# Performance work log

Measured on AMD Instinct MI355X. Metric: run time of the kernel, lower is better.

Reference implementation:

```python
import jax, jax.numpy as jnp
import numpy as np

N_NODES = 40962
N_EDGES = 245760
K = 10  # gaussian kernels
D = 2   # pseudo-coordinate dim
EPS = 1e-15


def gmm_conv(x, edge_index, pseudo, g, mu, sigma, root, bias):
    """PyG GMMConv with aggr='mean', root_weight=True.
    x: [N, Cin], edge_index: [2, E] (row 0 = source j, row 1 = target i),
    pseudo: [E, D], g: [Cin, K*Cout], mu/sigma: [K, D], root: [Cin, Cout], bias: [Cout].
    """
    src, dst = edge_index[0], edge_index[1]
    E = pseudo.shape[0]
    # Gaussian mixture edge weights: [E, K]
    diff = pseudo[:, None, :] - mu[None, :, :]                     # [E, K, D]
    w = jnp.exp(jnp.sum(-0.5 * diff * diff / (EPS + sigma[None] ** 2), axis=-1))
    xj = x[src]                                                    # [E, Cin] gather
    y = (xj @ g).reshape(E, K, -1)                                 # [E, K, Cout]
    msg = jnp.sum(y * w[:, :, None], axis=1)                       # [E, Cout]
    agg = jax.ops.segment_sum(msg, dst, num_segments=N_NODES)      # scatter-add
    deg = jax.ops.segment_sum(jnp.ones((E,), x.dtype), dst, num_segments=N_NODES)
    agg = agg / jnp.maximum(deg, 1.0)[:, None]                     # mean aggregation
    return agg + x @ root + bias


def setup_inputs() -> dict:
    key = jax.random.key(0)
    ks = jax.random.split(key, 20)
    Cin, Ch, Cout = 64, 64, 128
    sc = lambda fan: 1.0 / np.sqrt(fan)
    inp = {
        "x": jax.random.normal(ks[0], (N_NODES, Cin), jnp.float32),
        "edge_index": jax.random.randint(ks[1], (2, N_EDGES), 0, N_NODES, jnp.int32),
        "pseudo": jax.random.uniform(ks[2], (N_EDGES, D), jnp.float32),
        # conv1: Cin -> Ch
        "g1": jax.random.normal(ks[3], (Cin, K * Ch), jnp.float32) * sc(Cin),
        "mu1": jax.random.uniform(ks[4], (K, D), jnp.float32),
        "sigma1": jax.random.uniform(ks[5], (K, D), jnp.float32) + 0.5,
        "root1": jax.random.normal(ks[6], (Cin, Ch), jnp.float32) * sc(Cin),
        "b1": jnp.zeros((Ch,), jnp.float32),
        # conv2: Ch -> Cout
        "g2": jax.random.normal(ks[7], (Ch, K * Cout), jnp.float32) * sc(Ch),
        "mu2": jax.random.uniform(ks[8], (K, D), jnp.float32),
        "sigma2": jax.random.uniform(ks[9], (K, D), jnp.float32) + 0.5,
        "root2": jax.random.normal(ks[10], (Ch, Cout), jnp.float32) * sc(Ch),
        "b2": jnp.zeros((Cout,), jnp.float32),
        # shortcut: Cin -> Cout (size_in != size_out)
        "gs": jax.random.normal(ks[11], (Cin, K * Cout), jnp.float32) * sc(Cin),
        "mus": jax.random.uniform(ks[12], (K, D), jnp.float32),
        "sigmas": jax.random.uniform(ks[13], (K, D), jnp.float32) + 0.5,
        "roots": jax.random.normal(ks[14], (Cin, Cout), jnp.float32) * sc(Cin),
        "bs": jnp.zeros((Cout,), jnp.float32),
    }
    return inp


def reference(x, edge_index, pseudo, g1, mu1, sigma1, root1, b1,
              g2, mu2, sigma2, root2, b2, gs, mus, sigmas, roots, bs):
    h = gmm_conv(x, edge_index, pseudo, g1, mu1, sigma1, root1, b1)
    h = jax.nn.relu(h)
    y = gmm_conv(h, edge_index, pseudo, g2, mu2, sigma2, root2, b2)
    x_s = gmm_conv(x, edge_index, pseudo, gs, mus, sigmas, roots, bs)
    return jax.nn.relu(y + x_s)
```

## Files before the change

### kernel.cpp

```cpp
#include <hip/hip_runtime.h>
#include <hip/hip_bf16.h>

using bf16 = __hip_bfloat16;
typedef __attribute__((ext_vector_type(8))) short short8;
typedef __attribute__((ext_vector_type(4))) float float4v;

#define N_NODES 40962
#define N_EDGES 245760
#define NP      41024
#define KG      10
#define SCAN_B  256
#define NBLK    ((NP + SCAN_B - 1) / SCAN_B)
#define GRID1   (NP / 64)

#define CVT_V   (N_NODES * 64 / 8)
#define CVT_BLK ((CVT_V + 255) / 256)
#define W3_BLK  (N_EDGES / 256)
#define PACK_N  (64 * 704 + 2 * 128 * 704)
#define PACK_BLK (PACK_N / 256)


__device__ __forceinline__ float ldf(const void* p, size_t i, int isf32) {
    return isf32 ? ((const float*)p)[i] : __bfloat162float(((const bf16*)p)[i]);
}
__device__ __forceinline__ float blo(unsigned u) { return __uint_as_float(u << 16); }
__device__ __forceinline__ float bhi(unsigned u) { return __uint_as_float(u & 0xffff0000u); }
__device__ __forceinline__ unsigned pk2(float a, float b) {
    union { bf16 h[2]; unsigned u; } t;
    t.h[0] = __float2bfloat16(a);
    t.h[1] = __float2bfloat16(b);
    return t.u;
}

__global__ void k_detect_count(const void* x, const int* __restrict__ ei,
                               int* __restrict__ flag, int* __restrict__ deg) {
    if (blockIdx.x == 0) {
        __shared__ int huge_c, zero_even;
        if (threadIdx.x == 0) { huge_c = 0; zero_even = 0; }
        __syncthreads();
        const bf16* xb = (const bf16*)x;
        int lh = 0, lz = 0;
        for (int i = threadIdx.x; i < 8192; i += 256) {
            float v = __bfloat162float(xb[i]);
            if (!(fabsf(v) <= 1e4f)) lh++;
            if ((i & 1) == 0 && v == 0.0f) lz++;
        }
        atomicAdd(&huge_c, lh);
        atomicAdd(&zero_even, lz);
        __syncthreads();
        if (threadIdx.x == 0) flag[0] = (huge_c > 0 || zero_even > 3000) ? 1 : 0;
    } else {
        int e = (blockIdx.x - 1) * 256 + threadIdx.x;
        if (e < N_EDGES) atomicAdd(&deg[ei[N_EDGES + e]], 1);
    }
}

__global__ void k_scan1(const int* __restrict__ deg, int* __restrict__ offs,
                        int* __restrict__ bsum) {
    __shared__ int buf[SCAN_B];
    int t = threadIdx.x, b = blockIdx.x;
    int i = b * SCAN_B + t;
    int v = (i < NP) ? deg[i] : 0;
    buf[t] = v;
    __syncthreads();
    for (int off = 1; off < SCAN_B; off <<= 1) {
        int a = (t >= off) ? buf[t - off] : 0;
        __syncthreads();
        buf[t] += a;
        __syncthreads();
    }
    if (i < NP) offs[i] = buf[t] - v;
    if (t == SCAN_B - 1) bsum[b] = buf[t];
}

__global__ void k_scan2(const int* __restrict__ bsum, int* __restrict__ bofs,
                        int* __restrict__ total) {
    __shared__ int buf[256];
    int t = threadIdx.x;
    int v = (t < NBLK) ? bsum[t] : 0;
    buf[t] = v;
    __syncthreads();
    for (int off = 1; off < 256; off <<= 1) {
        int a = (t >= off) ? buf[t - off] : 0;
        __syncthreads();
        buf[t] += a;
        __syncthreads();
    }
    if (t < NBLK) bofs[t] = buf[t] - v;
    if (t == 255) total[0] = buf[255];
}

__global__ void k_scan3(int* __restrict__ offs, const int* __restrict__ bofs,
                        const int* __restrict__ total, const int* __restrict__ deg,
                        int* __restrict__ cur, float* __restrict__ invdeg) {
    int i = blockIdx.x * 256 + threadIdx.x;
    if (i < NP) {
        int o = offs[i] + bofs[i / SCAN_B];
        offs[i] = o;
        cur[i] = o;
        int d = deg[i];
        invdeg[i] = 1.0f / (float)(d > 1 ? d : 1);
    }
    if (i == 0) offs[NP] = total[0];
}

__global__ void k_fill(const int* __restrict__ ei, int* __restrict__ cur,
                       int* __restrict__ csr) {
    int e = blockIdx.x * 256 + threadIdx.x;
    if (e < N_EDGES) {
        int pos = atomicAdd(&cur[ei[N_EDGES + e]], 1);
        csr[pos] = e;
    }
}

__device__ __forceinline__ void gw_one(float p0, float p1, const void* mu,
                                       const void* sg, int f, float* out) {
#pragma unroll
    for (int k = 0; k < KG; k++) {
        float m0 = ldf(mu, 2 * k + 0, f), m1 = ldf(mu, 2 * k + 1, f);
        float s0 = ldf(sg, 2 * k + 0, f), s1 = ldf(sg, 2 * k + 1, f);
        float d0 = p0 - m0, d1 = p1 - m1;
        float t = -0.5f * (d0 * d0 / (1e-15f + s0 * s0) + d1 * d1 / (1e-15f + s1 * s1));
        out[k] = __expf(t);
    }
}

__device__ __forceinline__ void pack_frag(const void* g, const void* root, int f,
                                          int idx, int Cout, bf16* Bp) {
    int j = idx & 7;
    int lane = (idx >> 3) & 63;
    int rem = idx >> 9;
    int kc = rem % 22;
    int n = rem / 22;
    int col = n * 16 + (lane & 15);
    int k = kc * 32 + (lane >> 4) * 8 + j;
    float v;
    if (k < 512) {
        int cin = k >> 3, kg = k & 7;
        v = ldf(g, (size_t)cin * (KG * Cout) + (size_t)kg * Cout + col, f);
    } else if (k < 640) {
        int jj = k - 512;
        int cin = jj >> 1, kg = 8 + (jj & 1);
        v = ldf(g, (size_t)cin * (KG * Cout) + (size_t)kg * Cout + col, f);
    } else {
        v = ldf(root, (size_t)(k - 640) * Cout + col, f);
    }
    Bp[idx] = __float2bfloat16(v);
}

__global__ void k_prep_all(const void* __restrict__ x, const void* __restrict__ pseudo,
                           const void* mu1, const void* sg1, const void* mu2,
                           const void* sg2, const void* mus, const void* sgs,
                           const void* g1, const void* root1, const void* g2,
                           const void* root2, const void* gs, const void* roots,
                           const int* __restrict__ flag, bf16* __restrict__ Xf,
                           bf16* __restrict__ wab, bf16* __restrict__ w2b,
                           bf16* wt1p, bf16* wt2p, bf16* wtsp) {
    int b = blockIdx.x;
    int tid = threadIdx.x;
    int f = flag[0];
    if (b < CVT_BLK) {
        int i = b * 256 + tid;
        if (i < CVT_V) {
            int node = i >> 3, j = i & 7;
            uint4 u;
            if (f) {
                const float4* xf = (const float4*)x;
                float4 a = xf[2 * i], c = xf[2 * i + 1];
                union { bf16 t[8]; uint4 u; } tt;
                tt.t[0] = __float2bfloat16(a.x); tt.t[1] = __float2bfloat16(a.y);
                tt.t[2] = __float2bfloat16(a.z); tt.t[3] = __float2bfloat16(a.w);
                tt.t[4] = __float2bfloat16(c.x); tt.t[5] = __float2bfloat16(c.y);
                tt.t[6] = __float2bfloat16(c.z); tt.t[7] = __float2bfloat16(c.w);
                u = tt.u;
            } else {
                u = ((const uint4*)x)[i];
            }
            *(uint4*)(Xf + ((size_t)(j >> 2) * NP + node) * 32 + (j & 3) * 8) = u;
        }
    } else if (b < CVT_BLK + W3_BLK) {
        int e = (b - CVT_BLK) * 256 + tid;
        float p0 = ldf(pseudo, (size_t)e * 2 + 0, f);
        float p1 = ldf(pseudo, (size_t)e * 2 + 1, f);
        float o1[KG], o2[KG], os[KG];
        gw_one(p0, p1, mu1, sg1, f, o1);
        gw_one(p0, p1, mu2, sg2, f, o2);
        gw_one(p0, p1, mus, sgs, f, os);
        unsigned* d = (unsigned*)(wab + (size_t)e * 20);
        d[0] = pk2(o1[0], o1[1]); d[1] = pk2(o1[2], o1[3]);
        d[2] = pk2(o1[4], o1[5]); d[3] = pk2(o1[6], o1[7]);
        d[4] = pk2(o1[8], o1[9]);
        d[5] = pk2(os[0], os[1]); d[6] = pk2(os[2], os[3]);
        d[7] = pk2(os[4], os[5]); d[8] = pk2(os[6], os[7]);
        d[9] = pk2(os[8], os[9]);
        unsigned* d2 = (unsigned*)(w2b + (size_t)e * 10);
        d2[0] = pk2(o2[0], o2[1]); d2[1] = pk2(o2[2], o2[3]);
        d2[2] = pk2(o2[4], o2[5]); d2[3] = pk2(o2[6], o2[7]);
        d2[4] = pk2(o2[8], o2[9]);
    } else {
        int idx = (b - CVT_BLK - W3_BLK) * 256 + tid;
        if (idx < 64 * 704) {
            pack_frag(g1, root1, f, idx, 64, wt1p);
        } else if (idx < 64 * 704 + 128 * 704) {
            pack_frag(g2, root2, f, idx - 64 * 704, 128, wt2p);
        } else {
            pack_frag(gs, roots, f, idx - 64 * 704 - 128 * 704, 128, wtsp);
        }
    }
}

__device__ __forceinline__ void store_zf(bf16* Zf, int wid, int lane, const float* a,
                                         float inv) {
    union { bf16 h[8]; uint4 u; } p;
#pragma unroll
    for (int k = 0; k < 8; k++) p.h[k] = __float2bfloat16(a[k] * inv);
    *(uint4*)(Zf + ((size_t)(lane >> 2) * NP + wid) * 32 + (lane & 3) * 8) = p.u;
    *(unsigned*)(Zf + ((size_t)(16 + (lane >> 4)) * NP + wid) * 32 + (lane & 15) * 2) =
        pk2(a[8] * inv, a[9] * inv);
}

__device__ __forceinline__ float ldx_frag(const bf16* X, int src, int lane) {
    return __bfloat162float(X[((size_t)(lane >> 5) * NP + src) * 32 + (lane & 31)]);
}

__global__ void k_gather2(const int* __restrict__ ei, const int* __restrict__ offs,
                          const int* __restrict__ csr, const bf16* __restrict__ wab,
                          const float* __restrict__ invdeg, const bf16* __restrict__ X,
                          bf16* __restrict__ Za, bf16* __restrict__ Zb) {
    int wid = (blockIdx.x * 256 + threadIdx.x) >> 6;
    int lane = threadIdx.x & 63;
    if (wid >= NP) return;
    float aa[KG], ab[KG];
#pragma unroll
    for (int k = 0; k < KG; k++) { aa[k] = 0.0f; ab[k] = 0.0f; }
    int beg = __builtin_amdgcn_readfirstlane(offs[wid]);
    int end = __builtin_amdgcn_readfirstlane(offs[wid + 1]);
    for (int t = beg; t < end; ++t) {
        int e   = __builtin_amdgcn_readfirstlane(csr[t]);
        int src = __builtin_amdgcn_readfirstlane(ei[e]);
        const unsigned* wr = (const unsigned*)(wab + (size_t)e * 20);
        unsigned u0 = wr[0], u1 = wr[1], u2 = wr[2], u3 = wr[3], u4 = wr[4];
        unsigned v0 = wr[5], v1 = wr[6], v2 = wr[7], v3 = wr[8], v4 = wr[9];
        float xv = ldx_frag(X, src, lane);
        aa[0] += blo(u0) * xv; aa[1] += bhi(u0) * xv;
        aa[2] += blo(u1) * xv; aa[3] += bhi(u1) * xv;
        aa[4] += blo(u2) * xv; aa[5] += bhi(u2) * xv;
        aa[6] += blo(u3) * xv; aa[7] += bhi(u3) * xv;
        aa[8] += blo(u4) * xv; aa[9] += bhi(u4) * xv;
        ab[0] += blo(v0) * xv; ab[1] += bhi(v0) * xv;
        ab[2] += blo(v1) * xv; ab[3] += bhi(v1) * xv;
        ab[4] += blo(v2) * xv; ab[5] += bhi(v2) * xv;
        ab[6] += blo(v3) * xv; ab[7] += bhi(v3) * xv;
        ab[8] += blo(v4) * xv; ab[9] += bhi(v4) * xv;
    }
    float inv = invdeg[wid];
    store_zf(Za, wid, lane, aa, inv);
    store_zf(Zb, wid, lane, ab, inv);
}

__global__ void k_gather(const int* __restrict__ ei, const int* __restrict__ offs,
                         const int* __restrict__ csr, const bf16* __restrict__ w,
                         int wstride, const float* __restrict__ invdeg,
                         const bf16* __restrict__ X, bf16* __restrict__ Z) {
    int wid = (blockIdx.x * 256 + threadIdx.x) >> 6;
    int lane = threadIdx.x & 63;
    if (wid >= NP) return;
    float acc[KG];
#pragma unroll
    for (int k = 0; k < KG; k++) acc[k] = 0.0f;
    int beg = __builtin_amdgcn_readfirstlane(offs[wid]);
    int end = __builtin_amdgcn_readfirstlane(offs[wid + 1]);
    for (int t = beg; t < end; ++t) {
        int e   = __builtin_amdgcn_readfirstlane(csr[t]);
        int src = __builtin_amdgcn_readfirstlane(ei[e]);
        const unsigned* wr = (const unsigned*)(w + (size_t)e * wstride);
        unsigned u0 = wr[0], u1 = wr[1], u2 = wr[2], u3 = wr[3], u4 = wr[4];
        float xv = ldx_frag(X, src, lane);
        acc[0] += blo(u0) * xv; acc[1] += bhi(u0) * xv;
        acc[2] += blo(u1) * xv; acc[3] += bhi(u1) * xv;
        acc[4] += blo(u2) * xv; acc[5] += bhi(u2) * xv;
        acc[6] += blo(u3) * xv; acc[7] += bhi(u3) * xv;
        acc[8] += blo(u4) * xv; acc[9] += bhi(u4) * xv;
    }
    store_zf(Z, wid, lane, acc, invdeg[wid]);
}

template <int NT, int MODE>
__device__ __forceinline__ void gemm_body(
    int bid, const bf16* __restrict__ Zf, const bf16* __restrict__ Xf,
    const bf16* __restrict__ Bp, const void* __restrict__ bias, int f,
    const bf16* __restrict__ addsrc, bf16* __restrict__ outb,
    void* __restrict__ outp) {
    constexpr int Cout = NT * 16;
    int lane = threadIdx.x & 63;
    int wave = threadIdx.x >> 6;
    int m = lane & 15, quad = lane >> 4;
    int row0 = bid * 64 + wave * 16;

    const bf16* bbase = Bp + (size_t)lane * 8;
    const bf16* arow = Zf + ((size_t)(row0 + m)) * 32 + quad * 8;
    const bf16* xrow = Xf + ((size_t)(row0 + m)) * 32 + quad * 8;

    float4v acc[NT];
#pragma unroll
    for (int n = 0; n < NT; n++) acc[n] = (float4v){0.f, 0.f, 0.f, 0.f};

    short8 apre[4];
#pragma unroll
    for (int i = 0; i < 4; i++)
        apre[i] = *(const short8*)(arow + (size_t)i * NP * 32);
    short8 bcur[NT];
#pragma unroll
    for (int n = 0; n < NT; n++)
        bcur[n] = *(const short8*)(bbase + (size_t)(n * 22 + 0) * 512);

#pragma unroll
    for (int kc = 0; kc < 22; kc++) {
        short8 a = apre[kc & 3];
        int kn = kc + 4;
        if (kn < 22) {
            apre[kc & 3] = (kn < 20)
                ? *(const short8*)(arow + (size_t)kn * NP * 32)
                : *(const short8*)(xrow + (size_t)(kn - 20) * NP * 32);
        }
        short8 bnxt[NT];
        if (kc + 1 < 22) {
#pragma unroll
            for (int n = 0; n < NT; n++)
                bnxt[n] = *(const short8*)(bbase + (size_t)(n * 22 + kc + 1) * 512);
        }
#pragma unroll
        for (int n = 0; n < NT; n++)
            acc[n] = __builtin_amdgcn_mfma_f32_16x16x32_bf16(a, bcur[n], acc[n], 0, 0, 0);
        if (kc + 1 < 22) {
#pragma unroll
            for (int n = 0; n < NT; n++) bcur[n] = bnxt[n];
        }
    }

#pragma unroll
    for (int n = 0; n < NT; n++) {
        int gcol = n * 16 + m;
        float bv = ldf(bias, gcol, f);
#pragma unroll
        for (int r = 0; r < 4; r++) {
            int grow = row0 + quad * 4 + r;
            if (grow >= N_NODES) continue;
            float v = acc[n][r] + bv;
            if (MODE == 0) {
                outb[((size_t)(gcol >> 5) * NP + grow) * 32 + (gcol & 31)] =
                    __float2bfloat16(fmaxf(v, 0.f));
            } else if (MODE == 1) {
                outb[(size_t)grow * Cout + gcol] = __float2bfloat16(v);
            } else {
                size_t oidx = (size_t)grow * Cout + gcol;
                v = fmaxf(v + __bfloat162float(addsrc[oidx]), 0.f);
                if (f) ((float*)outp)[oidx] = v;
                else   ((bf16*)outp)[oidx] = __float2bfloat16(v);
            }
        }
    }
}

__global__ __launch_bounds__(256) void k_gemm_pair(
    const bf16* __restrict__ za, const bf16* __restrict__ zb,
    const bf16* __restrict__ Xf, const bf16* __restrict__ wt1p,
    const bf16* __restrict__ wtsp, const void* __restrict__ b1,
    const void* __restrict__ bs, const int* __restrict__ flag,
    bf16* __restrict__ hf, bf16* __restrict__ ys) {
    int f = flag[0];
    if (blockIdx.x < GRID1)
        gemm_body<4, 0>(blockIdx.x, za, Xf, wt1p, b1, f, nullptr, hf, nullptr);
    else
        gemm_body<8, 1>(blockIdx.x - GRID1, zb, Xf, wtsp, bs, f, nullptr, ys, nullptr);
}

template <int NT, int MODE>
__global__ __launch_bounds__(256) void k_gemm_one(
    const bf16* __restrict__ Zf, const bf16* __restrict__ Xf,
    const bf16* __restrict__ Bp, const void* __restrict__ bias,
    const int* __restrict__ flag, const bf16* __restrict__ addsrc,
    bf16* __restrict__ outb, void* __restrict__ outp) {
    gemm_body<NT, MODE>(blockIdx.x, Zf, Xf, Bp, bias, flag[0], addsrc, outb, outp);
}

extern "C" void kernel_launch(void* const* d_in, const int* in_sizes, int n_in,
                              void* d_out, int out_size, void* d_ws, size_t ws_size,
                              hipStream_t stream) {
    const void* x      = d_in[0];
    const int*  ei     = (const int*)d_in[1];
    const void* pseudo = d_in[2];
    const void* g1     = d_in[3];
    const void* mu1    = d_in[4];
    const void* sg1    = d_in[5];
    const void* root1  = d_in[6];
    const void* b1     = d_in[7];
    const void* g2     = d_in[8];
    const void* mu2    = d_in[9];
    const void* sg2    = d_in[10];
    const void* root2  = d_in[11];
    const void* b2     = d_in[12];
    const void* gs     = d_in[13];
    const void* mus    = d_in[14];
    const void* sgs    = d_in[15];
    const void* roots  = d_in[16];
    const void* bs     = d_in[17];

    char* ws = (char*)d_ws;
    size_t off = 0;
    auto alloc = [&](size_t bytes) -> char* {
        char* p = ws + off;
        off += (bytes + 255) & ~(size_t)255;
        return p;
    };
    const size_t ZSZ = (size_t)20 * NP * 32 * 2;
    const size_t XFS = (size_t)2 * NP * 32 * 2;

    int*   flag   = (int*)alloc(256);
    int*   deg    = (int*)alloc((size_t)NP * 4);
    int*   offs   = (int*)alloc((size_t)(NP + 1) * 4);
    int*   cur    = (int*)alloc((size_t)NP * 4);
    float* invdeg = (float*)alloc((size_t)NP * 4);
    int*   bsum   = (int*)alloc((size_t)NBLK * 4);
    int*   bofs   = (int*)alloc((size_t)NBLK * 4);
    int*   total  = (int*)alloc(256);
    int*   csr    = (int*)alloc((size_t)N_EDGES * 4);
    bf16*  Xf     = (bf16*)alloc(XFS);
    bf16*  hf     = (bf16*)alloc(XFS);
    bf16*  ys     = (bf16*)alloc((size_t)N_NODES * 128 * 2);
    bf16*  wt1p   = (bf16*)alloc((size_t)64 * 704 * 2);
    bf16*  wt2p   = (bf16*)alloc((size_t)128 * 704 * 2);
    bf16*  wtsp   = (bf16*)alloc((size_t)128 * 704 * 2);
    bf16*  wab    = (bf16*)alloc((size_t)N_EDGES * 20 * 2);
    bf16*  w2b    = (bf16*)alloc((size_t)N_EDGES * 10 * 2);
    size_t common_end = off;

    bf16* za = (bf16*)alloc(ZSZ);
    bf16* zb = (bf16*)alloc(ZSZ);
    bool big = (off <= ws_size);

    hipMemsetAsync(deg, 0, (size_t)NP * 4, stream);
    k_detect_count<<<1 + (N_EDGES + 255) / 256, 256, 0, stream>>>(x, ei, flag, deg);
    k_prep_all<<<CVT_BLK + W3_BLK + PACK_BLK, 256, 0, stream>>>(
        x, pseudo, mu1, sg1, mu2, sg2, mus, sgs, g1, root1, g2, root2, gs, roots,
        flag, Xf, wab, w2b, wt1p, wt2p, wtsp);
    k_scan1<<<NBLK, SCAN_B, 0, stream>>>(deg, offs, bsum);
    k_scan2<<<1, 256, 0, stream>>>(bsum, bofs, total);
    k_scan3<<<(NP + 255) / 256, 256, 0, stream>>>(offs, bofs, total, deg, cur, invdeg);
    k_fill<<<(N_EDGES + 255) / 256, 256, 0, stream>>>(ei, cur, csr);

    if (big) {
        k_gather2<<<NP / 4, 256, 0, stream>>>(ei, offs, csr, wab, invdeg, Xf, za, zb);
        k_gemm_pair<<<2 * GRID1, 256, 0, stream>>>(za, zb, Xf, wt1p, wtsp, b1, bs,
                                                   flag, hf, ys);
        k_gather<<<NP / 4, 256, 0, stream>>>(ei, offs, csr, w2b, 10, invdeg, hf, za);
        k_gemm_one<8, 2><<<GRID1, 256, 0, stream>>>(za, hf, wt2p, b2, flag, ys,
                                                    (bf16*)nullptr, d_out);
    } else {
        off = common_end;
        bf16* z = (bf16*)alloc(ZSZ);
        k_gather<<<NP / 4, 256, 0, stream>>>(ei, offs, csr, wab, 20, invdeg, Xf, z);
        k_gemm_one<4, 0><<<GRID1, 256, 0, stream>>>(z, Xf, wt1p, b1, flag,
                                                    (const bf16*)nullptr, hf, nullptr);
        k_gather<<<NP / 4, 256, 0, stream>>>(ei, offs, csr, wab + 10, 20, invdeg, Xf, z);
        k_gemm_one<8, 1><<<GRID1, 256, 0, stream>>>(z, Xf, wtsp, bs, flag,
                                                    (const bf16*)nullptr, ys, nullptr);
        k_gather<<<NP / 4, 256, 0, stream>>>(ei, offs, csr, w2b, 10, invdeg, hf, z);
        k_gemm_one<8, 2><<<GRID1, 256, 0, stream>>>(z, hf, wt2p, b2, flag, ys,
                                                    (bf16*)nullptr, d_out);
    }
}
```

Measured before the change: 312.4 us.

## Software-pipeline CSR gather loops and merge scan phases into one kernel

The gather kernels now prefetch edge ids, source indices, Gaussian weights and source features two or three edges ahead, rotating them through registers so the dependent chain of global loads (csr, then ei, then X) overlaps with the accumulation. Out-of-range prefetch indices are clamped so the extra loads stay in bounds. Separately, the second and third scan phases are fused: every block redundantly scans the block sums and applies its own offset, which saves one kernel launch. The cost is more live registers in the gather kernels and a few wasted loads past the end of each node's edge list.

```diff
diff --git a/kernel.cpp b/kernel.cpp
--- a/kernel.cpp
+++ b/kernel.cpp
@@ -31,6 +31,7 @@
     t.h[1] = __float2bfloat16(b);
     return t.u;
 }
+__device__ __forceinline__ int rfl(int v) { return __builtin_amdgcn_readfirstlane(v); }
 
 __global__ void k_detect_count(const void* x, const int* __restrict__ ei,
                                int* __restrict__ flag, int* __restrict__ deg) {
@@ -73,10 +74,11 @@
     if (t == SCAN_B - 1) bsum[b] = buf[t];
 }
 
-__global__ void k_scan2(const int* __restrict__ bsum, int* __restrict__ bofs,
-                        int* __restrict__ total) {
+__global__ void k_scan3m(int* __restrict__ offs, const int* __restrict__ bsum,
+                         const int* __restrict__ deg, int* __restrict__ cur,
+                         float* __restrict__ invdeg) {
     __shared__ int buf[256];
-    int t = threadIdx.x;
+    int t = threadIdx.x, b = blockIdx.x;
     int v = (t < NBLK) ? bsum[t] : 0;
     buf[t] = v;
     __syncthreads();
@@ -86,22 +88,17 @@
         buf[t] += a;
         __syncthreads();
     }
-    if (t < NBLK) bofs[t] = buf[t] - v;
-    if (t == 255) total[0] = buf[255];
-}
-
-__global__ void k_scan3(int* __restrict__ offs, const int* __restrict__ bofs,
-                        const int* __restrict__ total, const int* __restrict__ deg,
-                        int* __restrict__ cur, float* __restrict__ invdeg) {
-    int i = blockIdx.x * 256 + threadIdx.x;
+    int bofs = (b > 0) ? buf[b - 1] : 0;
+    int total = buf[NBLK - 1];
+    int i = b * 256 + t;
     if (i < NP) {
-        int o = offs[i] + bofs[i / SCAN_B];
+        int o = offs[i] + bofs;
         offs[i] = o;
         cur[i] = o;
         int d = deg[i];
         invdeg[i] = 1.0f / (float)(d > 1 ? d : 1);
     }
-    if (i == 0) offs[NP] = total[0];
+    if (i == 0) offs[NP] = total;
 }
 
 __global__ void k_fill(const int* __restrict__ ei, int* __restrict__ cur,
@@ -223,6 +220,11 @@
     return __bfloat162float(X[((size_t)(lane >> 5) * NP + src) * 32 + (lane & 31)]);
 }
 
+__device__ __forceinline__ int csr_at(const int* csr, int idx) {
+    if (idx > N_EDGES - 1) idx = N_EDGES - 1;
+    return rfl(csr[idx]);
+}
+
 __global__ void k_gather2(const int* __restrict__ ei, const int* __restrict__ offs,
                           const int* __restrict__ csr, const bf16* __restrict__ wab,
                           const float* __restrict__ invdeg, const bf16* __restrict__ X,
@@ -233,25 +235,45 @@
     float aa[KG], ab[KG];
 #pragma unroll
     for (int k = 0; k < KG; k++) { aa[k] = 0.0f; ab[k] = 0.0f; }
-    int beg = __builtin_amdgcn_readfirstlane(offs[wid]);
-    int end = __builtin_amdgcn_readfirstlane(offs[wid + 1]);
-    for (int t = beg; t < end; ++t) {
-        int e   = __builtin_amdgcn_readfirstlane(csr[t]);
-        int src = __builtin_amdgcn_readfirstlane(ei[e]);
-        const unsigned* wr = (const unsigned*)(wab + (size_t)e * 20);
-        unsigned u0 = wr[0], u1 = wr[1], u2 = wr[2], u3 = wr[3], u4 = wr[4];
-        unsigned v0 = wr[5], v1 = wr[6], v2 = wr[7], v3 = wr[8], v4 = wr[9];
-        float xv = ldx_frag(X, src, lane);
-        aa[0] += blo(u0) * xv; aa[1] += bhi(u0) * xv;
-        aa[2] += blo(u1) * xv; aa[3] += bhi(u1) * xv;
-        aa[4] += blo(u2) * xv; aa[5] += bhi(u2) * xv;
-        aa[6] += blo(u3) * xv; aa[7] += bhi(u3) * xv;
-        aa[8] += blo(u4) * xv; aa[9] += bhi(u4) * xv;
-        ab[0] += blo(v0) * xv; ab[1] += bhi(v0) * xv;
-        ab[2] += blo(v1) * xv; ab[3] += bhi(v1) * xv;
-        ab[4] += blo(v2) * xv; ab[5] += bhi(v2) * xv;
-        ab[6] += blo(v3) * xv; ab[7] += bhi(v3) * xv;
-        ab[8] += blo(v4) * xv; ab[9] += bhi(v4) * xv;
+    int beg = rfl(offs[wid]);
+    int end = rfl(offs[wid + 1]);
+    int cnt = end - beg;
+
+    int e0 = csr_at(csr, beg + 0);
+    int e1 = csr_at(csr, beg + 1);
+    int e2 = csr_at(csr, beg + 2);
+    int s1 = rfl(ei[e1]);
+    const unsigned* wp0 = (const unsigned*)(wab + (size_t)e0 * 20);
+    unsigned c0 = wp0[0], c1 = wp0[1], c2 = wp0[2], c3 = wp0[3], c4 = wp0[4];
+    unsigned c5 = wp0[5], c6 = wp0[6], c7 = wp0[7], c8 = wp0[8], c9 = wp0[9];
+    const unsigned* wp1 = (const unsigned*)(wab + (size_t)e1 * 20);
+    unsigned n0 = wp1[0], n1 = wp1[1], n2 = wp1[2], n3 = wp1[3], n4 = wp1[4];
+    unsigned n5 = wp1[5], n6 = wp1[6], n7 = wp1[7], n8 = wp1[8], n9 = wp1[9];
+    int s0 = rfl(ei[e0]);
+    float xv = ldx_frag(X, s0, lane);
+
+    for (int t = 0; t < cnt; ++t) {
+        int e3 = csr_at(csr, beg + t + 3);
+        int s2 = rfl(ei[e2]);
+        const unsigned* wp2 = (const unsigned*)(wab + (size_t)e2 * 20);
+        unsigned m0 = wp2[0], m1 = wp2[1], m2 = wp2[2], m3 = wp2[3], m4 = wp2[4];
+        unsigned m5 = wp2[5], m6 = wp2[6], m7 = wp2[7], m8 = wp2[8], m9 = wp2[9];
+        float xv1 = ldx_frag(X, s1, lane);
+        aa[0] += blo(c0) * xv; aa[1] += bhi(c0) * xv;
+        aa[2] += blo(c1) * xv; aa[3] += bhi(c1) * xv;
+        aa[4] += blo(c2) * xv; aa[5] += bhi(c2) * xv;
+        aa[6] += blo(c3) * xv; aa[7] += bhi(c3) * xv;
+        aa[8] += blo(c4) * xv; aa[9] += bhi(c4) * xv;
+        ab[0] += blo(c5) * xv; ab[1] += bhi(c5) * xv;
+        ab[2] += blo(c6) * xv; ab[3] += bhi(c6) * xv;
+        ab[4] += blo(c7) * xv; ab[5] += bhi(c7) * xv;
+        ab[6] += blo(c8) * xv; ab[7] += bhi(c8) * xv;
+        ab[8] += blo(c9) * xv; ab[9] += bhi(c9) * xv;
+        e2 = e3; s1 = s2; xv = xv1;
+        c0 = n0; c1 = n1; c2 = n2; c3 = n3; c4 = n4;
+        c5 = n5; c6 = n6; c7 = n7; c8 = n8; c9 = n9;
+        n0 = m0; n1 = m1; n2 = m2; n3 = m3; n4 = m4;
+        n5 = m5; n6 = m6; n7 = m7; n8 = m8; n9 = m9;
     }
     float inv = invdeg[wid];
     store_zf(Za, wid, lane, aa, inv);
@@ -268,19 +290,35 @@
     float acc[KG];
 #pragma unroll
     for (int k = 0; k < KG; k++) acc[k] = 0.0f;
-    int beg = __builtin_amdgcn_readfirstlane(offs[wid]);
-    int end = __builtin_amdgcn_readfirstlane(offs[wid + 1]);
-    for (int t = beg; t < end; ++t) {
-        int e   = __builtin_amdgcn_readfirstlane(csr[t]);
-        int src = __builtin_amdgcn_readfirstlane(ei[e]);
-        const unsigned* wr = (const unsigned*)(w + (size_t)e * wstride);
-        unsigned u0 = wr[0], u1 = wr[1], u2 = wr[2], u3 = wr[3], u4 = wr[4];
-        float xv = ldx_frag(X, src, lane);
-        acc[0] += blo(u0) * xv; acc[1] += bhi(u0) * xv;
-        acc[2] += blo(u1) * xv; acc[3] += bhi(u1) * xv;
-        acc[4] += blo(u2) * xv; acc[5] += bhi(u2) * xv;
-        acc[6] += blo(u3) * xv; acc[7] += bhi(u3) * xv;
-        acc[8] += blo(u4) * xv; acc[9] += bhi(u4) * xv;
+    int beg = rfl(offs[wid]);
+    int end = rfl(offs[wid + 1]);
+    int cnt = end - beg;
+
+    int e0 = csr_at(csr, beg + 0);
+    int e1 = csr_at(csr, beg + 1);
+    int e2 = csr_at(csr, beg + 2);
+    int s1 = rfl(ei[e1]);
+    const unsigned* wp0 = (const unsigned*)(w + (size_t)e0 * wstride);
+    unsigned c0 = wp0[0], c1 = wp0[1], c2 = wp0[2], c3 = wp0[3], c4 = wp0[4];
+    const unsigned* wp1 = (const unsigned*)(w + (size_t)e1 * wstride);
+    unsigned n0 = wp1[0], n1 = wp1[1], n2 = wp1[2], n3 = wp1[3], n4 = wp1[4];
+    int s0 = rfl(ei[e0]);
+    float xv = ldx_frag(X, s0, lane);
+
+    for (int t = 0; t < cnt; ++t) {
+        int e3 = csr_at(csr, beg + t + 3);
+        int s2 = rfl(ei[e2]);
+        const unsigned* wp2 = (const unsigned*)(w + (size_t)e2 * wstride);
+        unsigned m0 = wp2[0], m1 = wp2[1], m2 = wp2[2], m3 = wp2[3], m4 = wp2[4];
+        float xv1 = ldx_frag(X, s1, lane);
+        acc[0] += blo(c0) * xv; acc[1] += bhi(c0) * xv;
+        acc[2] += blo(c1) * xv; acc[3] += bhi(c1) * xv;
+        acc[4] += blo(c2) * xv; acc[5] += bhi(c2) * xv;
+        acc[6] += blo(c3) * xv; acc[7] += bhi(c3) * xv;
+        acc[8] += blo(c4) * xv; acc[9] += bhi(c4) * xv;
+        e2 = e3; s1 = s2; xv = xv1;
+        c0 = n0; c1 = n1; c2 = n2; c3 = n3; c4 = n4;
+        n0 = m0; n1 = m1; n2 = m2; n3 = m3; n4 = m4;
     }
     store_zf(Z, wid, lane, acc, invdeg[wid]);
 }
@@ -422,8 +460,6 @@
     int*   cur    = (int*)alloc((size_t)NP * 4);
     float* invdeg = (float*)alloc((size_t)NP * 4);
     int*   bsum   = (int*)alloc((size_t)NBLK * 4);
-    int*   bofs   = (int*)alloc((size_t)NBLK * 4);
-    int*   total  = (int*)alloc(256);
     int*   csr    = (int*)alloc((size_t)N_EDGES * 4);
     bf16*  Xf     = (bf16*)alloc(XFS);
     bf16*  hf     = (bf16*)alloc(XFS);
@@ -445,8 +481,7 @@
         x, pseudo, mu1, sg1, mu2, sg2, mus, sgs, g1, root1, g2, root2, gs, roots,
         flag, Xf, wab, w2b, wt1p, wt2p, wtsp);
     k_scan1<<<NBLK, SCAN_B, 0, stream>>>(deg, offs, bsum);
-    k_scan2<<<1, 256, 0, stream>>>(bsum, bofs, total);
-    k_scan3<<<(NP + 255) / 256, 256, 0, stream>>>(offs, bofs, total, deg, cur, invdeg);
+    k_scan3m<<<NBLK, 256, 0, stream>>>(offs, bsum, deg, cur, invdeg);
     k_fill<<<(N_EDGES + 255) / 256, 256, 0, stream>>>(ei, cur, csr);
 
     if (big) {
```

Result: faster. 298.7 us (-4.4%).
